# Kernel tuning notes

Hardware: AMD Instinct MI355X
Metric: run time of the kernel (lower is better)

Reference implementation:

```python
import jax, jax.numpy as jnp
import numpy as np

COST_CLASS, COST_BBOX, COST_GIOU = 1.0, 5.0, 2.0
NUM_FRAMES, Q_PER_FRAME, NUM_TGT, NUM_CLASSES = 36, 100, 20, 92
B = 64


def box_cxcywh_to_xyxy(b):
    cx, cy, w, h = b[..., 0], b[..., 1], b[..., 2], b[..., 3]
    return jnp.stack([cx - 0.5 * w, cy - 0.5 * h, cx + 0.5 * w, cy + 0.5 * h], axis=-1)


def pairwise_giou(b1, b2):
    # b1: [..., Q, 4], b2: [..., T, 4], xyxy -> giou [..., Q, T]
    area1 = (b1[..., 2] - b1[..., 0]) * (b1[..., 3] - b1[..., 1])
    area2 = (b2[..., 2] - b2[..., 0]) * (b2[..., 3] - b2[..., 1])
    lt = jnp.maximum(b1[..., :, None, :2], b2[..., None, :, :2])
    rb = jnp.minimum(b1[..., :, None, 2:], b2[..., None, :, 2:])
    wh = jnp.clip(rb - lt, 0.0)
    inter = wh[..., 0] * wh[..., 1]
    union = area1[..., :, None] + area2[..., None, :] - inter
    iou = inter / union
    lt_e = jnp.minimum(b1[..., :, None, :2], b2[..., None, :, :2])
    rb_e = jnp.maximum(b1[..., :, None, 2:], b2[..., None, :, 2:])
    wh_e = jnp.clip(rb_e - lt_e, 0.0)
    area_e = wh_e[..., 0] * wh_e[..., 1]
    return iou - (area_e - union) / area_e


def compute_cost(pred_logits, pred_boxes, tgt_labels, tgt_boxes):
    b = pred_logits.shape[0]
    prob = jax.nn.softmax(pred_logits.reshape(b, NUM_FRAMES, Q_PER_FRAME, -1), axis=-1)  # [B,F,Q,C]
    pb = pred_boxes.reshape(b, NUM_FRAMES, Q_PER_FRAME, 4)
    lab = jnp.transpose(tgt_labels, (1, 0, 2))            # [B,F,T]
    tb = jnp.transpose(tgt_boxes, (1, 0, 2, 3))           # [B,F,T,4]
    onehot = jax.nn.one_hot(lab, prob.shape[-1], dtype=prob.dtype)  # [B,F,T,C]
    cost_class = -jnp.einsum('bfqc,bftc->bfqt', prob, onehot)
    cost_bbox = jnp.abs(pb[:, :, :, None, :] - tb[:, :, None, :, :]).sum(-1)  # L1 cdist
    giou = pairwise_giou(box_cxcywh_to_xyxy(pb), box_cxcywh_to_xyxy(tb))
    return COST_CLASS * cost_class + COST_BBOX * cost_bbox - COST_GIOU * giou


def auction_assign(cost):
    # cost [Q, T]; returns obj_of [T]: query index assigned to each target.
    # eps-optimal auction algorithm (replaces scipy linear_sum_assignment).
    Q, T = cost.shape
    benefit = -cost.T  # [T, Q]
    spread = jnp.max(benefit) - jnp.min(benefit) + 1e-6
    eps = spread / 1000.0
    neg_inf = jnp.asarray(-1e30, cost.dtype)

    def cond(s):
        _, _, obj_of, it = s
        return jnp.logical_and(jnp.any(obj_of < 0), it < 20000)

    def body(s):
        price, owner, obj_of, it = s
        unassigned = obj_of < 0                       # [T]
        vals = benefit - price[None, :]               # [T, Q]
        top2v, top2i = jax.lax.top_k(vals, 2)
        best_obj = top2i[:, 0]                        # [T]
        bid = price[best_obj] + (top2v[:, 0] - top2v[:, 1]) + eps
        bid = jnp.where(unassigned, bid, neg_inf)
        best_bid = jnp.full((Q,), neg_inf, cost.dtype).at[best_obj].max(bid)
        pids = jnp.arange(T, dtype=jnp.int32)
        win = unassigned & (bid >= best_bid[best_obj])
        winner = jnp.full((Q,), T, jnp.int32).at[best_obj].min(jnp.where(win, pids, T))
        has_bid = winner < T
        # evict previous owners of objects that received a bid
        evict = jnp.where(has_bid & (owner >= 0), owner, T)
        obj_of = obj_of.at[evict].set(-1, mode='drop')
        qids = jnp.arange(Q, dtype=jnp.int32)
        obj_of = obj_of.at[jnp.where(has_bid, winner, T)].set(jnp.where(has_bid, qids, -1), mode='drop')
        price = jnp.where(has_bid, best_bid, price)
        owner = jnp.where(has_bid, winner, owner)
        return price, owner, obj_of, it + 1

    init = (jnp.zeros((Q,), cost.dtype), jnp.full((Q,), -1, jnp.int32),
            jnp.full((T,), -1, jnp.int32), jnp.int32(0))
    _, _, obj_of, _ = jax.lax.while_loop(cond, body, init)
    return obj_of


def setup_inputs() -> dict:
    key = jax.random.key(0)
    k1, k2, k3, k4 = jax.random.split(key, 4)
    pred_logits = jax.random.normal(k1, (B, NUM_FRAMES * Q_PER_FRAME, NUM_CLASSES), jnp.float32)
    pred_boxes = jax.random.uniform(k2, (B, NUM_FRAMES * Q_PER_FRAME, 4), jnp.float32)
    tgt_labels = jax.random.randint(k3, (NUM_FRAMES, B, NUM_TGT), 0, NUM_CLASSES, jnp.int32)
    tgt_boxes = jax.random.uniform(k4, (NUM_FRAMES, B, NUM_TGT, 4), jnp.float32)
    return {'pred_logits': pred_logits, 'pred_boxes': pred_boxes,
            'tgt_labels': tgt_labels, 'tgt_boxes': tgt_boxes}


def reference(pred_logits, pred_boxes, tgt_labels, tgt_boxes):
    cost = compute_cost(pred_logits, pred_boxes, tgt_labels, tgt_boxes)  # [B,F,Q,T]
    b, f, q, t = cost.shape
    obj_of = jax.vmap(auction_assign)(cost.reshape(b * f, q, t))  # [BF, T]
    order = jnp.argsort(obj_of, axis=-1)  # scipy returns rows ascending
    pred_idx = jnp.take_along_axis(obj_of, order, axis=-1).reshape(b, f, t)
    tgt_idx = order.astype(jnp.int32).reshape(b, f, t)
    return cost, pred_idx, tgt_idx
```

## Files before the change

### kernel.cpp

```cpp
#include <hip/hip_runtime.h>

#define NF 36
#define QN 100
#define TN 20
#define CN 92
#define NB 64
#define BSTR 112

#define SCAN6(BV, PV, IDX) do { \
    float v_ = (BV) - (PV); \
    bool c_ = v_ > v0; \
    bool d_ = v_ > v1; \
    float nv1_ = __builtin_amdgcn_fmed3f(v_, v0, v1); \
    i1 = c_ ? i0 : (d_ ? (IDX) : i1); \
    b1 = c_ ? b0 : (d_ ? (BV) : b1); \
    v1 = nv1_; \
    i0 = c_ ? (IDX) : i0; \
    b0 = c_ ? (BV) : b0; \
    v0 = fmaxf(v0, v_); } while (0)

#define MERGE6(NV0, NI0, NB0, NV1, NI1, NB1) do { \
    bool t_  = (NV0) > v0; \
    bool s1_ = (NV1) > v0; \
    bool s2_ = (NV0) > v1; \
    float mv1_ = t_ ? (s1_ ? (NV1) : v0) : (s2_ ? (NV0) : v1); \
    int   mi1_ = t_ ? (s1_ ? (NI1) : i0) : (s2_ ? (NI0) : i1); \
    float mb1_ = t_ ? (s1_ ? (NB1) : b0) : (s2_ ? (NB0) : b1); \
    v0 = t_ ? (NV0) : v0; \
    i0 = t_ ? (NI0) : i0; \
    b0 = t_ ? (NB0) : b0; \
    v1 = mv1_; i1 = mi1_; b1 = mb1_; } while (0)

__global__ __launch_bounds__(64) void matcher_kernel(
    const float* __restrict__ logits,
    const float* __restrict__ pboxes,
    const int*   __restrict__ tlabels,
    const float* __restrict__ tboxes,
    float* __restrict__ out_cost,
    float* __restrict__ out_pred,
    float* __restrict__ out_tgt)
{
    const int bf = blockIdx.x;
    const int b  = bf / NF;
    const int f  = bf % NF;
    const int lane = threadIdx.x;

    __shared__ __align__(16) float ben[TN][BSTR];
    __shared__ __align__(16) float price[BSTR];
    __shared__ unsigned long long bid2[TN];
    __shared__ int   objl[TN];
    __shared__ int   slab[TN];
    __shared__ float tbr[TN][4];
    __shared__ float tbx[TN][4];
    __shared__ float tarea[TN];

    if (lane < TN) {
        const int base = (f * NB + b) * TN + lane;
        slab[lane] = tlabels[base];
        const float* tb = tboxes + (size_t)base * 4;
        float cx = tb[0], cy = tb[1], w = tb[2], h = tb[3];
        tbr[lane][0] = cx; tbr[lane][1] = cy; tbr[lane][2] = w; tbr[lane][3] = h;
        float x1 = cx - 0.5f * w, y1 = cy - 0.5f * h;
        float x2 = cx + 0.5f * w, y2 = cy + 0.5f * h;
        tbx[lane][0] = x1; tbx[lane][1] = y1; tbx[lane][2] = x2; tbx[lane][3] = y2;
        tarea[lane] = (x2 - x1) * (y2 - y1);
    }
    __syncthreads();

    float mn = INFINITY, mx = -INFINITY;
    for (int p = 0; p < 2; ++p) {
        const int q = lane + 64 * p;
        if (q < QN) {
            const size_t row = (size_t)b * (NF * QN) + (size_t)f * QN + q;
            const float* L = logits + row * CN;
            const float4* L4 = reinterpret_cast<const float4*>(L);
            float4 r[23];
            #pragma unroll
            for (int i = 0; i < 23; ++i) r[i] = L4[i];
            #pragma unroll
            for (int i = 0; i < 23; ++i) {
                asm volatile("" : "+v"(r[i].x), "+v"(r[i].y), "+v"(r[i].z), "+v"(r[i].w));
            }
            float m = -INFINITY;
            #pragma unroll
            for (int i = 0; i < 23; ++i) {
                float4 v = r[i];
                m = fmaxf(m, v.x); m = fmaxf(m, v.y); m = fmaxf(m, v.z); m = fmaxf(m, v.w);
            }
            float s = 0.f;
            #pragma unroll
            for (int i = 0; i < 23; ++i) {
                float4 v = r[i];
                s += expf(v.x - m); s += expf(v.y - m); s += expf(v.z - m); s += expf(v.w - m);
            }

            float4 pbv = reinterpret_cast<const float4*>(pboxes)[row];
            float cx = pbv.x, cy = pbv.y, w = pbv.z, h = pbv.w;
            float px1 = cx - 0.5f * w, py1 = cy - 0.5f * h;
            float px2 = cx + 0.5f * w, py2 = cy + 0.5f * h;
            float a1 = (px2 - px1) * (py2 - py1);

            for (int t = 0; t < TN; ++t) {
                float pc = expf(L[slab[t]] - m) / s;
                float cb = fabsf(cx - tbr[t][0]) + fabsf(cy - tbr[t][1]);
                cb = cb + fabsf(w - tbr[t][2]);
                cb = cb + fabsf(h - tbr[t][3]);
                float ltx = fmaxf(px1, tbx[t][0]), lty = fmaxf(py1, tbx[t][1]);
                float rbx = fminf(px2, tbx[t][2]), rby = fminf(py2, tbx[t][3]);
                float wx = fmaxf(rbx - ltx, 0.f), wy = fmaxf(rby - lty, 0.f);
                float inter = wx * wy;
                float uni = a1 + tarea[t] - inter;
                float iou = inter / uni;
                float ex1 = fminf(px1, tbx[t][0]), ey1 = fminf(py1, tbx[t][1]);
                float ex2 = fmaxf(px2, tbx[t][2]), ey2 = fmaxf(py2, tbx[t][3]);
                float ew = fmaxf(ex2 - ex1, 0.f), eh = fmaxf(ey2 - ey1, 0.f);
                float ae = ew * eh;
                float giou = iou - (ae - uni) / ae;
                float cost = (-pc) + 5.0f * cb - 2.0f * giou;
                ben[t][q] = -cost;
                mn = fminf(mn, cost);
                mx = fmaxf(mx, cost);
            }
        }
    }

    for (int i = lane; i < BSTR; i += 64) price[i] = 0.f;
    if (lane < TN) {
        float4 ninf; ninf.x = ninf.y = ninf.z = ninf.w = -INFINITY;
        float4* sp = reinterpret_cast<float4*>(&ben[lane][100]);
        sp[0] = ninf; sp[1] = ninf; sp[2] = ninf;
    }
    __syncthreads();

    #pragma unroll
    for (int off = 32; off > 0; off >>= 1) {
        mn = fminf(mn, __shfl_xor(mn, off, 64));
        mx = fmaxf(mx, __shfl_xor(mx, off, 64));
    }
    const float eps = (((-mn) - (-mx)) + 1e-6f) / 1000.0f;

    {
        float4* dst = reinterpret_cast<float4*>(out_cost + (size_t)bf * (QN * TN));
        for (int i = lane; i < (QN * TN) / 4; i += 64) {
            int k = i * 4;
            int q = k / TN, t0 = k - q * TN;
            float4 v;
            v.x = -ben[t0 + 0][q]; v.y = -ben[t0 + 1][q];
            v.z = -ben[t0 + 2][q]; v.w = -ben[t0 + 3][q];
            dst[i] = v;
        }
    }

    const int myt = lane / 3;
    const int jj  = lane - myt * 3;
    const int q0  = jj * 36;
    const bool is_leader = (lane < 60) && (jj == 0);
    float4 breg4[9];
    {
        const int tt = (lane < 60) ? myt : 0;
        const float4* bp = reinterpret_cast<const float4*>(&ben[tt][q0]);
        #pragma unroll
        for (int k = 0; k < 9; ++k) breg4[k] = bp[k];
    }
    int myobj = -1;

    float cv0 = 0.f, cv1 = 0.f, cb0 = 0.f, cb1 = 0.f, cp0 = 0.f;
    int ci0 = 0, ci1 = 0;
    bool cval = false;

    for (int it = 0; it < 20000; ++it) {
        unsigned long long U = __ballot(is_leader && (myobj < 0));
        if (U == 0ull) break;
        unsigned long long R = __ballot(is_leader && (myobj < 0) && !cval);

        if (R != 0ull) {
            const bool doscan = (lane < 60) && (((R >> (3 * myt)) & 1ull) != 0ull);
            float v0 = -INFINITY, v1 = -INFINITY, b0 = 0.f, b1 = 0.f;
            int i0 = q0, i1 = q0;
            if (doscan) {
                const float4* pp = reinterpret_cast<const float4*>(&price[q0]);
                #pragma unroll
                for (int k = 0; k < 9; ++k) {
                    float4 bv = breg4[k];
                    float4 pv = pp[k];
                    SCAN6(bv.x, pv.x, q0 + 4*k + 0);
                    SCAN6(bv.y, pv.y, q0 + 4*k + 1);
                    SCAN6(bv.z, pv.z, q0 + 4*k + 2);
                    SCAN6(bv.w, pv.w, q0 + 4*k + 3);
                }
            }
            {
                float av0 = __shfl_down(v0, 1), av1 = __shfl_down(v1, 1);
                float ab0 = __shfl_down(b0, 1), ab1 = __shfl_down(b1, 1);
                int   ai0 = __shfl_down(i0, 1), ai1 = __shfl_down(i1, 1);
                float bv0 = __shfl_down(v0, 2), bv1 = __shfl_down(v1, 2);
                float bb0 = __shfl_down(b0, 2), bb1 = __shfl_down(b1, 2);
                int   bi0 = __shfl_down(i0, 2), bi1 = __shfl_down(i1, 2);
                MERGE6(av0, ai0, ab0, av1, ai1, ab1);
                MERGE6(bv0, bi0, bb0, bv1, bi1, bb1);
            }
            if (is_leader && (((R >> lane) & 1ull) != 0ull)) {
                cv0 = v0; ci0 = i0; cb0 = b0;
                cv1 = v1; ci1 = i1; cb1 = b1;
                cp0 = price[ci0];
                cval = true;
            }
        }

        const bool active = is_leader && (myobj < 0);
        const int   mybidq = ci0;
        const float mybid  = cp0 + (cv0 - cv1) + eps;
        if (active) {
            bid2[myt] = ((unsigned long long)__float_as_uint(mybid) << 32) | (unsigned)mybidq;
        }

        if (is_leader) {
            bool lose = false, hit0 = false, kill = false, ev = false;
            float np0 = -INFINITY;
            unsigned long long uu = U;
            while (uu) {
                int pos = (int)__builtin_ctzll(uu); uu &= uu - 1ull;
                int t2 = pos / 3;
                unsigned long long pk = bid2[t2];
                int q2 = (int)(unsigned)(pk & 0xffffffffull);
                float f2 = __uint_as_float((unsigned)(pk >> 32));
                lose = lose || (active && q2 == mybidq &&
                                (f2 > mybid || (f2 == mybid && t2 < myt)));
                ev = ev || (q2 == myobj);
                bool h0 = (q2 == ci0);
                np0 = h0 ? fmaxf(np0, f2) : np0;
                hit0 = hit0 || h0;
                kill = kill || (q2 == ci1);
            }
            if (active && !lose) {
                myobj = mybidq;
                price[mybidq] = mybid;
            } else if (ev) {
                myobj = -1;
            }
            if (cval) {
                if (hit0) { cp0 = np0; cv0 = cb0 - cp0; }
                if (kill || (hit0 && !(cv0 > cv1))) cval = false;
            }
        }
    }
    __syncthreads();
    if (is_leader) objl[myt] = myobj;
    __syncthreads();

    if (lane < TN) {
        int v = objl[lane];
        int r = 0;
        for (int u2 = 0; u2 < TN; ++u2) {
            int w = objl[u2];
            r += (w < v) || (w == v && u2 < lane);
        }
        out_pred[(size_t)bf * TN + r] = (float)v;
        out_tgt[(size_t)bf * TN + r]  = (float)lane;
    }
}

extern "C" void kernel_launch(void* const* d_in, const int* in_sizes, int n_in,
                              void* d_out, int out_size, void* d_ws, size_t ws_size,
                              hipStream_t stream) {
    const float* logits  = (const float*)d_in[0];
    const float* pboxes  = (const float*)d_in[1];
    const int*   tlabels = (const int*)d_in[2];
    const float* tboxes  = (const float*)d_in[3];

    float* out = (float*)d_out;
    float* out_cost = out;
    float* out_pred = out + (size_t)NB * NF * QN * TN;
    float* out_tgt  = out_pred + (size_t)NB * NF * TN;

    hipLaunchKernelGGL(matcher_kernel, dim3(NB * NF), dim3(64), 0, stream,
                       logits, pboxes, tlabels, tboxes, out_cost, out_pred, out_tgt);
}
```

Before: 184.7 us.

## Resolve auction bids with LDS atomicMax keys and top-3 cached candidates

Replaces the per-iteration serial loop in which each leader read every bidder's bid with a packed (price, target) 64-bit key per query, updated through atomicMax in shared memory. Ownership changes are then detected by comparing stored keys. Leaders cache the top three candidates instead of two, so a rescan is needed less often after price changes. Benefit values are now reread from LDS on each scan instead of held in registers, and the asm register pin on the logits is dropped. This adds atomic traffic and the correctness risk that comes with visibility and ordering inside a single wavefront.

```diff
diff --git a/kernel.cpp b/kernel.cpp
--- a/kernel.cpp
+++ b/kernel.cpp
@@ -7,29 +7,26 @@
 #define NB 64
 #define BSTR 112
 
-#define SCAN6(BV, PV, IDX) do { \
-    float v_ = (BV) - (PV); \
-    bool c_ = v_ > v0; \
-    bool d_ = v_ > v1; \
-    float nv1_ = __builtin_amdgcn_fmed3f(v_, v0, v1); \
-    i1 = c_ ? i0 : (d_ ? (IDX) : i1); \
-    b1 = c_ ? b0 : (d_ ? (BV) : b1); \
-    v1 = nv1_; \
-    i0 = c_ ? (IDX) : i0; \
-    b0 = c_ ? (BV) : b0; \
+#define SCAN3(VV, IDX) do { \
+    float v_ = (VV); \
+    bool c0_ = v_ > v0; \
+    bool c1_ = v_ > v1; \
+    bool c2_ = v_ > v2; \
+    i2 = c1_ ? i1 : (c2_ ? (IDX) : i2); \
+    v2 = __builtin_amdgcn_fmed3f(v_, v1, v2); \
+    i1 = c0_ ? i0 : (c1_ ? (IDX) : i1); \
+    v1 = __builtin_amdgcn_fmed3f(v_, v0, v1); \
+    i0 = c0_ ? (IDX) : i0; \
     v0 = fmaxf(v0, v_); } while (0)
 
-#define MERGE6(NV0, NI0, NB0, NV1, NI1, NB1) do { \
-    bool t_  = (NV0) > v0; \
-    bool s1_ = (NV1) > v0; \
-    bool s2_ = (NV0) > v1; \
-    float mv1_ = t_ ? (s1_ ? (NV1) : v0) : (s2_ ? (NV0) : v1); \
-    int   mi1_ = t_ ? (s1_ ? (NI1) : i0) : (s2_ ? (NI0) : i1); \
-    float mb1_ = t_ ? (s1_ ? (NB1) : b0) : (s2_ ? (NB0) : b1); \
-    v0 = t_ ? (NV0) : v0; \
-    i0 = t_ ? (NI0) : i0; \
-    b0 = t_ ? (NB0) : b0; \
-    v1 = mv1_; i1 = mi1_; b1 = mb1_; } while (0)
+#define CSWAP(VA,IA,BA,KA, VB,IB,BB,KB) do { \
+    bool sw_ = ((VB) > (VA)) || (((VB) == (VA)) && ((IB) < (IA))); \
+    float tv_ = sw_ ? (VB) : (VA); float uv_ = sw_ ? (VA) : (VB); (VA) = tv_; (VB) = uv_; \
+    int   ti_ = sw_ ? (IB) : (IA); int   ui_ = sw_ ? (IA) : (IB); (IA) = ti_; (IB) = ui_; \
+    float tb_ = sw_ ? (BB) : (BA); float ub_ = sw_ ? (BA) : (BB); (BA) = tb_; (BB) = ub_; \
+    unsigned long long tk_ = sw_ ? (KB) : (KA); \
+    unsigned long long uk_ = sw_ ? (KA) : (KB); (KA) = tk_; (KB) = uk_; \
+} while (0)
 
 __global__ __launch_bounds__(64) void matcher_kernel(
     const float* __restrict__ logits,
@@ -47,7 +44,7 @@
 
     __shared__ __align__(16) float ben[TN][BSTR];
     __shared__ __align__(16) float price[BSTR];
-    __shared__ unsigned long long bid2[TN];
+    __shared__ unsigned long long pk[BSTR];
     __shared__ int   objl[TN];
     __shared__ int   slab[TN];
     __shared__ float tbr[TN][4];
@@ -77,10 +74,6 @@
             float4 r[23];
             #pragma unroll
             for (int i = 0; i < 23; ++i) r[i] = L4[i];
-            #pragma unroll
-            for (int i = 0; i < 23; ++i) {
-                asm volatile("" : "+v"(r[i].x), "+v"(r[i].y), "+v"(r[i].z), "+v"(r[i].w));
-            }
             float m = -INFINITY;
             #pragma unroll
             for (int i = 0; i < 23; ++i) {
@@ -124,7 +117,7 @@
         }
     }
 
-    for (int i = lane; i < BSTR; i += 64) price[i] = 0.f;
+    for (int i = lane; i < BSTR; i += 64) { price[i] = 0.f; pk[i] = 0ull; }
     if (lane < TN) {
         float4 ninf; ninf.x = ninf.y = ninf.z = ninf.w = -INFINITY;
         float4* sp = reinterpret_cast<float4*>(&ben[lane][100]);
@@ -155,92 +148,86 @@
     const int jj  = lane - myt * 3;
     const int q0  = jj * 36;
     const bool is_leader = (lane < 60) && (jj == 0);
-    float4 breg4[9];
-    {
-        const int tt = (lane < 60) ? myt : 0;
-        const float4* bp = reinterpret_cast<const float4*>(&ben[tt][q0]);
-        #pragma unroll
-        for (int k = 0; k < 9; ++k) breg4[k] = bp[k];
-    }
     int myobj = -1;
-
-    float cv0 = 0.f, cv1 = 0.f, cb0 = 0.f, cb1 = 0.f, cp0 = 0.f;
-    int ci0 = 0, ci1 = 0;
+    unsigned long long my_key = 0ull;
+
+    float cv0 = 0.f, cv1 = 0.f, cv2 = 0.f, cb0 = 0.f, cb1 = 0.f, cb2 = 0.f, cB = 0.f;
+    int ci0 = 0, ci1 = 0, ci2 = 0;
+    unsigned long long ck0 = 0ull, ck1 = 0ull, ck2 = 0ull;
     bool cval = false;
 
     for (int it = 0; it < 20000; ++it) {
+        if (is_leader) {
+            if (myobj >= 0) {
+                if (pk[myobj] != my_key) myobj = -1;
+            }
+            if (cval) {
+                unsigned long long n0 = pk[ci0], n1 = pk[ci1], n2 = pk[ci2];
+                bool ch0 = (n0 != ck0), ch1 = (n1 != ck1), ch2 = (n2 != ck2);
+                if (ch0 | ch1 | ch2) {
+                    if (ch0) { ck0 = n0; cv0 = cb0 - __uint_as_float((unsigned)(n0 >> 32)); }
+                    if (ch1) { ck1 = n1; cv1 = cb1 - __uint_as_float((unsigned)(n1 >> 32)); }
+                    if (ch2) { ck2 = n2; cv2 = cb2 - __uint_as_float((unsigned)(n2 >> 32)); }
+                    CSWAP(cv0,ci0,cb0,ck0, cv1,ci1,cb1,ck1);
+                    CSWAP(cv1,ci1,cb1,ck1, cv2,ci2,cb2,ck2);
+                    CSWAP(cv0,ci0,cb0,ck0, cv1,ci1,cb1,ck1);
+                    cval = (cv0 > cB) && (cv1 >= cB);
+                }
+            }
+        }
+
         unsigned long long U = __ballot(is_leader && (myobj < 0));
         if (U == 0ull) break;
         unsigned long long R = __ballot(is_leader && (myobj < 0) && !cval);
 
         if (R != 0ull) {
             const bool doscan = (lane < 60) && (((R >> (3 * myt)) & 1ull) != 0ull);
-            float v0 = -INFINITY, v1 = -INFINITY, b0 = 0.f, b1 = 0.f;
-            int i0 = q0, i1 = q0;
+            float v0 = -INFINITY, v1 = -INFINITY, v2 = -INFINITY;
+            int i0 = q0, i1 = q0, i2 = q0;
             if (doscan) {
+                const int tt = myt;
                 const float4* pp = reinterpret_cast<const float4*>(&price[q0]);
+                const float4* bp = reinterpret_cast<const float4*>(&ben[tt][q0]);
                 #pragma unroll
                 for (int k = 0; k < 9; ++k) {
-                    float4 bv = breg4[k];
+                    float4 bv = bp[k];
                     float4 pv = pp[k];
-                    SCAN6(bv.x, pv.x, q0 + 4*k + 0);
-                    SCAN6(bv.y, pv.y, q0 + 4*k + 1);
-                    SCAN6(bv.z, pv.z, q0 + 4*k + 2);
-                    SCAN6(bv.w, pv.w, q0 + 4*k + 3);
+                    SCAN3(bv.x - pv.x, q0 + 4*k + 0);
+                    SCAN3(bv.y - pv.y, q0 + 4*k + 1);
+                    SCAN3(bv.z - pv.z, q0 + 4*k + 2);
+                    SCAN3(bv.w - pv.w, q0 + 4*k + 3);
                 }
             }
-            {
-                float av0 = __shfl_down(v0, 1), av1 = __shfl_down(v1, 1);
-                float ab0 = __shfl_down(b0, 1), ab1 = __shfl_down(b1, 1);
-                int   ai0 = __shfl_down(i0, 1), ai1 = __shfl_down(i1, 1);
-                float bv0 = __shfl_down(v0, 2), bv1 = __shfl_down(v1, 2);
-                float bb0 = __shfl_down(b0, 2), bb1 = __shfl_down(b1, 2);
-                int   bi0 = __shfl_down(i0, 2), bi1 = __shfl_down(i1, 2);
-                MERGE6(av0, ai0, ab0, av1, ai1, ab1);
-                MERGE6(bv0, bi0, bb0, bv1, bi1, bb1);
-            }
+            float sav0 = __shfl_down(v0, 1), sav1 = __shfl_down(v1, 1), sav2 = __shfl_down(v2, 1);
+            int   sai0 = __shfl_down(i0, 1), sai1 = __shfl_down(i1, 1), sai2 = __shfl_down(i2, 1);
+            float sbv0 = __shfl_down(v0, 2), sbv1 = __shfl_down(v1, 2), sbv2 = __shfl_down(v2, 2);
+            int   sbi0 = __shfl_down(i0, 2), sbi1 = __shfl_down(i1, 2), sbi2 = __shfl_down(i2, 2);
             if (is_leader && (((R >> lane) & 1ull) != 0ull)) {
-                cv0 = v0; ci0 = i0; cb0 = b0;
-                cv1 = v1; ci1 = i1; cb1 = b1;
-                cp0 = price[ci0];
+                SCAN3(sav0, sai0); SCAN3(sav1, sai1); SCAN3(sav2, sai2);
+                SCAN3(sbv0, sbi0); SCAN3(sbv1, sbi1); SCAN3(sbv2, sbi2);
+                ci0 = i0; ci1 = i1; ci2 = i2;
+                cv0 = v0; cv1 = v1; cv2 = v2; cB = v2;
+                cb0 = ben[myt][ci0]; cb1 = ben[myt][ci1]; cb2 = ben[myt][ci2];
+                ck0 = pk[ci0]; ck1 = pk[ci1]; ck2 = pk[ci2];
                 cval = true;
             }
         }
 
         const bool active = is_leader && (myobj < 0);
-        const int   mybidq = ci0;
-        const float mybid  = cp0 + (cv0 - cv1) + eps;
         if (active) {
-            bid2[myt] = ((unsigned long long)__float_as_uint(mybid) << 32) | (unsigned)mybidq;
-        }
-
-        if (is_leader) {
-            bool lose = false, hit0 = false, kill = false, ev = false;
-            float np0 = -INFINITY;
-            unsigned long long uu = U;
-            while (uu) {
-                int pos = (int)__builtin_ctzll(uu); uu &= uu - 1ull;
-                int t2 = pos / 3;
-                unsigned long long pk = bid2[t2];
-                int q2 = (int)(unsigned)(pk & 0xffffffffull);
-                float f2 = __uint_as_float((unsigned)(pk >> 32));
-                lose = lose || (active && q2 == mybidq &&
-                                (f2 > mybid || (f2 == mybid && t2 < myt)));
-                ev = ev || (q2 == myobj);
-                bool h0 = (q2 == ci0);
-                np0 = h0 ? fmaxf(np0, f2) : np0;
-                hit0 = hit0 || h0;
-                kill = kill || (q2 == ci1);
-            }
-            if (active && !lose) {
-                myobj = mybidq;
-                price[mybidq] = mybid;
-            } else if (ev) {
-                myobj = -1;
-            }
-            if (cval) {
-                if (hit0) { cp0 = np0; cv0 = cb0 - cp0; }
-                if (kill || (hit0 && !(cv0 > cv1))) cval = false;
+            float cp0 = __uint_as_float((unsigned)(ck0 >> 32));
+            float mybid = cp0 + (cv0 - cv1) + eps;
+            unsigned long long mykey =
+                ((unsigned long long)__float_as_uint(mybid) << 32) |
+                (unsigned long long)(63 - myt);
+            atomicMax(&pk[ci0], mykey);
+            bool win;
+            if ((U & (U - 1ull)) == 0ull) win = true;
+            else win = (pk[ci0] == mykey);
+            if (win) {
+                myobj = ci0;
+                my_key = mykey;
+                price[ci0] = mybid;
             }
         }
     }
```

After: 190.4 us. 3.1% more time.
